# Optimization experiments

Hardware: AMD Instinct MI355X
Metric: run time of the kernel (lower is better)

Reference implementation:

```python
import jax, jax.numpy as jnp
import numpy as np

B, S, D, H = 128, 200, 512, 8
DF = D // H  # per-head feature dim = 64
SCALE = np.float32(1.0 / np.sqrt(DF))
NEG_INF = np.float32(-1e32)


def setup_inputs() -> dict:
    key = jax.random.key(0)
    ks = jax.random.split(key, 8)
    xavier = np.float32(np.sqrt(6.0 / (D + D)))  # xavier_uniform_ bound for square Linear
    def lin_w(k):
        return jax.random.uniform(k, (D, D), jnp.float32, -xavier, xavier)
    return {
        "q": jax.random.normal(ks[0], (B, S, D), jnp.float32),
        "k": jax.random.normal(ks[1], (B, S, D), jnp.float32),
        "v": jax.random.normal(ks[2], (B, S, D), jnp.float32),
        "Wq": lin_w(ks[3]), "bq": jnp.zeros((D,), jnp.float32),
        "Wk": lin_w(ks[4]), "bk": jnp.zeros((D,), jnp.float32),
        "Wv": lin_w(ks[5]), "bv": jnp.zeros((D,), jnp.float32),
        "Wo": lin_w(ks[6]), "bo": jnp.zeros((D,), jnp.float32),
        # causal mask: attend only to positions <= query position
        "mask": jnp.tril(jnp.ones((1, 1, S, S), dtype=bool)),
        "zero_pad": 1,
    }


def reference(q, k, v, Wq, bq, Wk, bk, Wv, bv, Wo, bo, mask, zero_pad):
    bs, s, d = q.shape
    # QKV projections -> [B, H, S, DF]
    qh = (q @ Wq.T + bq).reshape(bs, s, H, DF).transpose(0, 2, 1, 3)
    kh = (k @ Wk.T + bk).reshape(bs, s, H, DF).transpose(0, 2, 1, 3)
    vh = (v @ Wv.T + bv).reshape(bs, s, H, DF).transpose(0, 2, 1, 3)
    # attention4dis_kt: scaled dot-product, causal mask fill with -1e32, softmax
    scores = jnp.einsum("bhqd,bhkd->bhqk", qh, kh) * SCALE
    scores = jnp.where(mask, scores, NEG_INF)
    attn = jax.nn.softmax(scores, axis=-1)  # [B, H, S, S]
    if zero_pad:
        # replace first query row of attention weights with zeros
        attn = attn.at[:, :, 0, :].set(0.0)
    # dropout is identity in eval mode
    out = jnp.einsum("bhqk,bhkd->bhqd", attn, vh)
    concat = out.transpose(0, 2, 1, 3).reshape(bs, s, d)
    return concat @ Wo.T + bo
```

## Files before the change

### kernel.cpp

```cpp
#include <hip/hip_runtime.h>
#include <hip/hip_bf16.h>

#define SEQ  200
#define DIM  512
#define NH   8
#define DF   64
#define SPAD 256
#define NEG  -1.0e30f

typedef __bf16 bf16x8 __attribute__((ext_vector_type(8)));
typedef __bf16 bf16x4 __attribute__((ext_vector_type(4)));
typedef float  f32x4  __attribute__((ext_vector_type(4)));

__device__ __forceinline__ void async_lds16(const void* g, void* l)
{
    __builtin_amdgcn_global_load_lds(
        (const __attribute__((address_space(1))) void*)g,
        (__attribute__((address_space(3))) void*)l, 16, 0, 0);
}

struct DetArgs { const unsigned short* p[11]; };

__global__ void detect_all(DetArgs a, int* __restrict__ flags)
{
    const unsigned short* __restrict__ src = a.p[blockIdx.x];
    __shared__ int cnt;
    if (threadIdx.x == 0) cnt = 0;
    __syncthreads();
    int ok = 0;
#pragma unroll
    for (int i = 0; i < 2; ++i) {
        const unsigned short u = src[threadIdx.x * 2 + i];
        const float f = __uint_as_float(((unsigned int)u) << 16);
        const float fa = fabsf(f);
        ok += (f == 0.0f) || (fa >= 6.0e-5f && fa <= 64.0f);
    }
    atomicAdd(&cnt, ok);
    __syncthreads();
    if (threadIdx.x == 0) flags[blockIdx.x] = (cnt < 448) ? 1 : 0;
}

struct CvtArgs { const void* src[8]; __bf16* dst[8]; };

__global__ void cvt_all(CvtArgs a, const int* __restrict__ flags)
{
    const int blk = blockIdx.x;
    int job; long idx, n8;
    if (blk < 512) { job = blk >> 7; idx = (long)(blk & 127) * 256 + threadIdx.x; n8 = (long)DIM * DIM / 8; }
    else           { job = 4 + (blk - 512); idx = threadIdx.x; n8 = DIM / 8; }
    if (idx >= n8) return;
    const int fl = flags[3 + job];
    if (fl) {
        const f32x4* s = (const f32x4*)a.src[job];
        const f32x4 x = s[2 * idx], y = s[2 * idx + 1];
        bf16x8 o;
        o[0] = (__bf16)x[0]; o[1] = (__bf16)x[1];
        o[2] = (__bf16)x[2]; o[3] = (__bf16)x[3];
        o[4] = (__bf16)y[0]; o[5] = (__bf16)y[1];
        o[6] = (__bf16)y[2]; o[7] = (__bf16)y[3];
        ((bf16x8*)a.dst[job])[idx] = o;
    } else {
        ((bf16x8*)a.dst[job])[idx] = ((const bf16x8*)a.src[job])[idx];
    }
}

template <int MODE, int USE_FLAG, typename OutT>
__global__ __launch_bounds__(256, 2)
void gemm_bt_kernel(const void* __restrict__ Araw, long m_off,
                    const __bf16* __restrict__ Bt,
                    const __bf16* __restrict__ bias,
                    OutT* __restrict__ C,
                    int M, int N, int K,
                    const int* __restrict__ flag)
{
    __shared__ __align__(16) __bf16 lA[2][128 * 32];
    __shared__ __align__(16) __bf16 lB[2][128 * 32];

    const int af32 = USE_FLAG ? flag[0] : 0;
    const __bf16* A16 = (const __bf16*)Araw;
    const float*  A32 = (const float*)Araw;

    const int tid  = threadIdx.x;
    const int m0   = blockIdx.x * 128;
    const int n0   = blockIdx.y * 128;
    const int w    = tid >> 6;
    const int lane = tid & 63;
    const int lr   = lane & 15, quad = lane >> 4;
    const int wm   = (w >> 1) * 64, wn = (w & 1) * 64;

    int srow[2], scol[2];
#pragma unroll
    for (int p = 0; p < 2; ++p) {
        const int e = (p * 256 + tid) * 8;
        srow[p] = e >> 5;
        scol[p] = e & 31;
    }

    const int KS = K >> 5;
    f32x4 rf[2][2];

#pragma unroll
    for (int p = 0; p < 2; ++p)
        async_lds16(Bt + (size_t)(n0 + srow[p]) * K + scol[p],
                    &lB[0][(p * 256 + tid) * 8]);
    if (af32) {
#pragma unroll
        for (int p = 0; p < 2; ++p) {
            const size_t aoff = (size_t)(m_off + m0 + srow[p]) * K + scol[p];
            rf[p][0] = *(const f32x4*)(A32 + aoff);
            rf[p][1] = *(const f32x4*)(A32 + aoff + 4);
        }
    } else {
#pragma unroll
        for (int p = 0; p < 2; ++p)
            async_lds16(A16 + (size_t)(m_off + m0 + srow[p]) * K + scol[p],
                        &lA[0][(p * 256 + tid) * 8]);
    }

    f32x4 acc[4][4] = {};

    for (int ks = 0; ks < KS; ++ks) {
        const int buf = ks & 1;

        if (af32) {
#pragma unroll
            for (int p = 0; p < 2; ++p) {
                bf16x8 o;
                o[0] = (__bf16)rf[p][0][0]; o[1] = (__bf16)rf[p][0][1];
                o[2] = (__bf16)rf[p][0][2]; o[3] = (__bf16)rf[p][0][3];
                o[4] = (__bf16)rf[p][1][0]; o[5] = (__bf16)rf[p][1][1];
                o[6] = (__bf16)rf[p][1][2]; o[7] = (__bf16)rf[p][1][3];
                *(bf16x8*)&lA[buf][(p * 256 + tid) * 8] = o;
            }
        }

        __syncthreads();

        if (ks + 1 < KS) {
            const int k1 = (ks + 1) * 32;
#pragma unroll
            for (int p = 0; p < 2; ++p)
                async_lds16(Bt + (size_t)(n0 + srow[p]) * K + k1 + scol[p],
                            &lB[buf ^ 1][(p * 256 + tid) * 8]);
            if (af32) {
#pragma unroll
                for (int p = 0; p < 2; ++p) {
                    const size_t aoff =
                        (size_t)(m_off + m0 + srow[p]) * K + k1 + scol[p];
                    rf[p][0] = *(const f32x4*)(A32 + aoff);
                    rf[p][1] = *(const f32x4*)(A32 + aoff + 4);
                }
            } else {
#pragma unroll
                for (int p = 0; p < 2; ++p)
                    async_lds16(A16 + (size_t)(m_off + m0 + srow[p]) * K + k1 + scol[p],
                                &lA[buf ^ 1][(p * 256 + tid) * 8]);
            }
        }

        bf16x8 af[4], bfr[4];
#pragma unroll
        for (int mi = 0; mi < 4; ++mi)
            af[mi] = *(const bf16x8*)&lA[buf][(wm + mi * 16 + lr) * 32 + quad * 8];
#pragma unroll
        for (int ni = 0; ni < 4; ++ni)
            bfr[ni] = *(const bf16x8*)&lB[buf][(wn + ni * 16 + lr) * 32 + quad * 8];
#pragma unroll
        for (int mi = 0; mi < 4; ++mi)
#pragma unroll
            for (int ni = 0; ni < 4; ++ni)
                acc[mi][ni] = __builtin_amdgcn_mfma_f32_16x16x32_bf16(
                    af[mi], bfr[ni], acc[mi][ni], 0, 0, 0);
    }

#pragma unroll
    for (int ni = 0; ni < 4; ++ni) {
        const int col = n0 + wn + ni * 16 + lr;
        const float bb = (float)bias[col];
        if constexpr (MODE == 2) {
            const int h = col >> 6, df = col & 63;
#pragma unroll
            for (int mi = 0; mi < 4; ++mi) {
                const int row0 = m0 + wm + mi * 16 + quad * 4;
                const int b = row0 / SEQ, s0 = row0 - b * SEQ;
                bf16x4 pk;
#pragma unroll
                for (int r = 0; r < 4; ++r)
                    pk[r] = (__bf16)(acc[mi][ni][r] + bb);
                *(bf16x4*)&C[(((size_t)(b * NH + h)) * DF + df) * SPAD + s0] = pk;
            }
        } else {
#pragma unroll
            for (int mi = 0; mi < 4; ++mi) {
#pragma unroll
                for (int r = 0; r < 4; ++r) {
                    const int row = m0 + wm + mi * 16 + quad * 4 + r;
                    const float vv = acc[mi][ni][r] + bb;
                    size_t addr;
                    if (MODE == 0) {
                        addr = (size_t)row * N + col;
                    } else {
                        const int b = row / SEQ, s = row - b * SEQ;
                        const int h = col >> 6, df = col & 63;
                        addr = (((size_t)(b * NH + h)) * SEQ + s) * DF + df;
                    }
                    C[addr] = (OutT)vv;
                }
            }
        }
    }
}

#define KROWS 208
#define KSTR  72
#define VSTR  232
#define PSTR  136

__global__ __launch_bounds__(256, 2)
void attn_mfma(const __bf16* __restrict__ Qh,
               const __bf16* __restrict__ Kh,
               const __bf16* __restrict__ Vt,
               __bf16* __restrict__ Ctx,
               const int* __restrict__ zp)
{
    __shared__ __align__(16) __bf16 Kl[KROWS * KSTR];
    __shared__ __align__(16) __bf16 Vl[DF * VSTR];
    __shared__ __align__(16) __bf16 Pl[4][16 * PSTR];

    const int tid  = threadIdx.x;
    const int w    = tid >> 6, lane = tid & 63;
    const int lr   = lane & 15, quad = lane >> 4;
    const int bh   = blockIdx.x;
    const int b    = bh >> 3, h = bh & 7;
    const size_t qkbase = (size_t)bh * SEQ * DF;
    const size_t vbase  = (size_t)bh * DF * SPAD;
    const int zero_pad = zp[0];

    for (int i = tid; i < (KROWS * DF) / 8; i += 256) {
        const int row = i >> 3, c8 = (i & 7) * 8;
        *(bf16x8*)&Kl[row * KSTR + c8] =
            *(const bf16x8*)(Kh + qkbase + (size_t)row * DF + c8);
    }
    for (int i = tid; i < (DF * 224) / 8; i += 256) {
        const int d = i / 28, kb = (i % 28) * 8;
        bf16x8 vv = {};
        if (kb < SEQ)
            vv = *(const bf16x8*)(Vt + vbase + (size_t)d * SPAD + kb);
        *(bf16x8*)&Vl[d * VSTR + kb] = vv;
    }
    __syncthreads();

    __bf16* pw = Pl[w];

    const unsigned int mine =
        (unsigned int)(0x0459F38AF17BF26CULL >> (16 * w)) & 0xFFFFu;

    for (int j = 0; j < 4; ++j) {
        const int qt = (mine >> (4 * j)) & 15;
        if (qt == 15) continue;
        const int q = qt * 16 + lr;

        bf16x8 qf0, qf1;
        {
            const __bf16* qp = Qh + qkbase + (size_t)(qt * 16 + lr) * DF + quad * 8;
            qf0 = *(const bf16x8*)qp;
            qf1 = *(const bf16x8*)(qp + 32);
        }

        f32x4 sc[14];
#pragma unroll
        for (int kt = 0; kt < 13; ++kt) {
            if (kt > qt) continue;
            const int krow = kt * 16 + lr;
            const bf16x8 kf0 = *(const bf16x8*)&Kl[krow * KSTR + quad * 8];
            const bf16x8 kf1 = *(const bf16x8*)&Kl[krow * KSTR + 32 + quad * 8];
            f32x4 z = {};
            z = __builtin_amdgcn_mfma_f32_16x16x32_bf16(kf0, qf0, z, 0, 0, 0);
            z = __builtin_amdgcn_mfma_f32_16x16x32_bf16(kf1, qf1, z, 0, 0, 0);
            sc[kt] = z;
        }

        float mx = NEG;
#pragma unroll
        for (int kt = 0; kt < 13; ++kt) {
            if (kt > qt) continue;
#pragma unroll
            for (int r = 0; r < 4; ++r) {
                const int kk = kt * 16 + quad * 4 + r;
                const float s = (kk <= q && kk < SEQ) ? sc[kt][r] * 0.125f : NEG;
                sc[kt][r] = s;
                mx = fmaxf(mx, s);
            }
        }
        mx = fmaxf(mx, __shfl_xor(mx, 16, 64));
        mx = fmaxf(mx, __shfl_xor(mx, 32, 64));

        float l = 0.0f;
#pragma unroll
        for (int kt = 0; kt < 13; ++kt) {
            if (kt > qt) continue;
#pragma unroll
            for (int r = 0; r < 4; ++r) {
                const float pv = __expf(sc[kt][r] - mx);
                sc[kt][r] = pv;
                l += pv;
            }
        }
        l += __shfl_xor(l, 16, 64);
        l += __shfl_xor(l, 32, 64);
        const float linv = 1.0f / l;

        f32x4 oacc[4] = {};

#pragma unroll
        for (int kt = 0; kt < 8; ++kt) {
            if (kt <= qt) {
                bf16x4 pkv;
#pragma unroll
                for (int r = 0; r < 4; ++r) pkv[r] = (__bf16)sc[kt][r];
                *(bf16x4*)&pw[lr * PSTR + kt * 16 + quad * 4] = pkv;
            } else if (kt == qt + 1) {
                *(bf16x4*)&pw[lr * PSTR + kt * 16 + quad * 4] = (bf16x4){};
            }
        }
#pragma unroll
        for (int c = 0; c < 4; ++c) {
            if (2 * c > qt) continue;
            const bf16x8 pf = *(const bf16x8*)&pw[lr * PSTR + c * 32 + quad * 8];
#pragma unroll
            for (int nt = 0; nt < 4; ++nt) {
                const bf16x8 vf =
                    *(const bf16x8*)&Vl[(nt * 16 + lr) * VSTR + c * 32 + quad * 8];
                oacc[nt] = __builtin_amdgcn_mfma_f32_16x16x32_bf16(
                    pf, vf, oacc[nt], 0, 0, 0);
            }
        }

        if (qt >= 8) {
#pragma unroll
            for (int kt = 8; kt < 14; ++kt) {
                if (kt <= qt) {
                    bf16x4 pkv;
#pragma unroll
                    for (int r = 0; r < 4; ++r) pkv[r] = (__bf16)sc[kt][r];
                    *(bf16x4*)&pw[lr * PSTR + (kt - 8) * 16 + quad * 4] = pkv;
                } else if (kt == qt + 1) {
                    *(bf16x4*)&pw[lr * PSTR + (kt - 8) * 16 + quad * 4] = (bf16x4){};
                }
            }
#pragma unroll
            for (int c = 0; c < 3; ++c) {
                if (2 * (c + 4) > qt) continue;
                const bf16x8 pf = *(const bf16x8*)&pw[lr * PSTR + c * 32 + quad * 8];
#pragma unroll
                for (int nt = 0; nt < 4; ++nt) {
                    const bf16x8 vf =
                        *(const bf16x8*)&Vl[(nt * 16 + lr) * VSTR + (c + 4) * 32 + quad * 8];
                    oacc[nt] = __builtin_amdgcn_mfma_f32_16x16x32_bf16(
                        pf, vf, oacc[nt], 0, 0, 0);
                }
            }
        }

        float il[4];
#pragma unroll
        for (int r = 0; r < 4; ++r) il[r] = __shfl(linv, quad * 4 + r, 16);
#pragma unroll
        for (int nt = 0; nt < 4; ++nt) {
            const int d = nt * 16 + lr;
#pragma unroll
            for (int r = 0; r < 4; ++r) {
                const int qq = qt * 16 + quad * 4 + r;
                if (qq < SEQ) {
                    float ov = oacc[nt][r] * il[r];
                    if (zero_pad && qq == 0) ov = 0.0f;
                    Ctx[((size_t)(b * SEQ + qq)) * DIM + h * DF + d] = (__bf16)ov;
                }
            }
        }
    }
}

extern "C" void kernel_launch(void* const* d_in, const int* in_sizes, int n_in,
                              void* d_out, int out_size, void* d_ws, size_t ws_size,
                              hipStream_t stream)
{
    const void* q  = d_in[0];
    const void* k  = d_in[1];
    const void* v  = d_in[2];
    const void* Ws[4] = {d_in[3], d_in[5], d_in[7], d_in[9]};
    const void* bs[4] = {d_in[4], d_in[6], d_in[8], d_in[10]};
    const int*  zp = (const int*)d_in[12];
    float* Out = (float*)d_out;

    int* flags = (int*)d_ws;
    __bf16* Wc[4]; __bf16* bc[4];
    __bf16* p = (__bf16*)((char*)d_ws + 256);
    for (int i = 0; i < 4; ++i) { Wc[i] = p; p += (size_t)DIM * DIM; }
    for (int i = 0; i < 4; ++i) { bc[i] = p; p += DIM; }
    const size_t fixed_bytes = (size_t)((char*)p - (char*)d_ws);

    const int B_total = 128;
    int cb = 128;
    while (cb > 16) {
        const size_t crows_t = (size_t)cb * SEQ;
        const size_t elems = 4 * crows_t * DIM + (size_t)cb * NH * DF * SPAD;
        if (fixed_bytes + elems * 2 <= ws_size) break;
        cb >>= 1;
    }
    const int nchunk = B_total / cb;
    const size_t crows = (size_t)cb * SEQ;
    const size_t celems = crows * DIM;

    __bf16* Qh  = p;
    __bf16* Kh  = Qh + celems;
    __bf16* Vt  = Kh + celems;
    __bf16* Ctx = Vt + (size_t)cb * NH * DF * SPAD;

    const dim3 blk(256);
    const dim3 g((unsigned)(crows / 128), DIM / 128);

    DetArgs da;
    da.p[0] = (const unsigned short*)q;
    da.p[1] = (const unsigned short*)k;
    da.p[2] = (const unsigned short*)v;
    for (int i = 0; i < 4; ++i) {
        da.p[3 + i] = (const unsigned short*)Ws[i];
        da.p[7 + i] = (const unsigned short*)bs[i];
    }
    detect_all<<<dim3(11), blk, 0, stream>>>(da, flags);

    CvtArgs ca;
    for (int i = 0; i < 4; ++i) {
        ca.src[i] = Ws[i];     ca.dst[i] = Wc[i];
        ca.src[4 + i] = bs[i]; ca.dst[4 + i] = bc[i];
    }
    cvt_all<<<dim3(516), blk, 0, stream>>>(ca, flags);

    for (int c = 0; c < nchunk; ++c) {
        const long moff = (long)c * (long)crows;
        gemm_bt_kernel<1, 1, __bf16><<<g, blk, 0, stream>>>(
            q, moff, Wc[0], bc[0], Qh, (int)crows, DIM, DIM, &flags[0]);
        gemm_bt_kernel<1, 1, __bf16><<<g, blk, 0, stream>>>(
            k, moff, Wc[1], bc[1], Kh, (int)crows, DIM, DIM, &flags[1]);
        gemm_bt_kernel<2, 1, __bf16><<<g, blk, 0, stream>>>(
            v, moff, Wc[2], bc[2], Vt, (int)crows, DIM, DIM, &flags[2]);
        attn_mfma<<<dim3(cb * NH), blk, 0, stream>>>(Qh, Kh, Vt, Ctx, zp);
        gemm_bt_kernel<0, 0, float><<<g, blk, 0, stream>>>(
            Ctx, 0, Wc[3], bc[3], Out + (size_t)c * celems,
            (int)crows, DIM, DIM, nullptr);
    }
}
```

Baseline: 329.7 us.

## Drop K staging in LDS and stream P in small chunks to raise occupancy

Removes the shared-memory copy of K. The attention kernel now reads K fragments straight from global memory, relying on L1/L2 caching across waves. It also replaces the large per-wave P buffer with a 16x40 buffer that is refilled for each 32-column chunk, which shrinks LDS use enough to raise the launch bound to 4 blocks per CU. The trade-off is more global/L2 traffic and latency for K, which is reread by up to 4 waves, plus more LDS write/read round trips per chunk.

```diff
diff --git a/kernel.cpp b/kernel.cpp
--- a/kernel.cpp
+++ b/kernel.cpp
@@ -211,21 +211,18 @@
     }
 }
 
-#define KROWS 208
-#define KSTR  72
 #define VSTR  232
-#define PSTR  136
-
-__global__ __launch_bounds__(256, 2)
+#define PSTRW 40
+
+__global__ __launch_bounds__(256, 4)
 void attn_mfma(const __bf16* __restrict__ Qh,
                const __bf16* __restrict__ Kh,
                const __bf16* __restrict__ Vt,
                __bf16* __restrict__ Ctx,
                const int* __restrict__ zp)
 {
-    __shared__ __align__(16) __bf16 Kl[KROWS * KSTR];
     __shared__ __align__(16) __bf16 Vl[DF * VSTR];
-    __shared__ __align__(16) __bf16 Pl[4][16 * PSTR];
+    __shared__ __align__(16) __bf16 Pl[4][16 * PSTRW];
 
     const int tid  = threadIdx.x;
     const int w    = tid >> 6, lane = tid & 63;
@@ -236,11 +233,6 @@
     const size_t vbase  = (size_t)bh * DF * SPAD;
     const int zero_pad = zp[0];
 
-    for (int i = tid; i < (KROWS * DF) / 8; i += 256) {
-        const int row = i >> 3, c8 = (i & 7) * 8;
-        *(bf16x8*)&Kl[row * KSTR + c8] =
-            *(const bf16x8*)(Kh + qkbase + (size_t)row * DF + c8);
-    }
     for (int i = tid; i < (DF * 224) / 8; i += 256) {
         const int d = i / 28, kb = (i % 28) * 8;
         bf16x8 vv = {};
@@ -267,13 +259,13 @@
             qf1 = *(const bf16x8*)(qp + 32);
         }
 
-        f32x4 sc[14];
+        f32x4 sc[13];
 #pragma unroll
         for (int kt = 0; kt < 13; ++kt) {
             if (kt > qt) continue;
-            const int krow = kt * 16 + lr;
-            const bf16x8 kf0 = *(const bf16x8*)&Kl[krow * KSTR + quad * 8];
-            const bf16x8 kf1 = *(const bf16x8*)&Kl[krow * KSTR + 32 + quad * 8];
+            const __bf16* kp = Kh + qkbase + (size_t)(kt * 16 + lr) * DF + quad * 8;
+            const bf16x8 kf0 = *(const bf16x8*)kp;
+            const bf16x8 kf1 = *(const bf16x8*)(kp + 32);
             f32x4 z = {};
             z = __builtin_amdgcn_mfma_f32_16x16x32_bf16(kf0, qf0, z, 0, 0, 0);
             z = __builtin_amdgcn_mfma_f32_16x16x32_bf16(kf1, qf1, z, 0, 0, 0);
@@ -311,54 +303,28 @@
         const float linv = 1.0f / l;
 
         f32x4 oacc[4] = {};
-
-#pragma unroll
-        for (int kt = 0; kt < 8; ++kt) {
-            if (kt <= qt) {
-                bf16x4 pkv;
-#pragma unroll
-                for (int r = 0; r < 4; ++r) pkv[r] = (__bf16)sc[kt][r];
-                *(bf16x4*)&pw[lr * PSTR + kt * 16 + quad * 4] = pkv;
-            } else if (kt == qt + 1) {
-                *(bf16x4*)&pw[lr * PSTR + kt * 16 + quad * 4] = (bf16x4){};
-            }
-        }
-#pragma unroll
-        for (int c = 0; c < 4; ++c) {
+#pragma unroll
+        for (int c = 0; c < 7; ++c) {
             if (2 * c > qt) continue;
-            const bf16x8 pf = *(const bf16x8*)&pw[lr * PSTR + c * 32 + quad * 8];
+#pragma unroll
+            for (int tt = 0; tt < 2; ++tt) {
+                const int t = 2 * c + tt;
+                if (t <= qt) {
+                    bf16x4 pkv;
+#pragma unroll
+                    for (int r = 0; r < 4; ++r) pkv[r] = (__bf16)sc[t][r];
+                    *(bf16x4*)&pw[lr * PSTRW + tt * 16 + quad * 4] = pkv;
+                } else if (t == qt + 1) {
+                    *(bf16x4*)&pw[lr * PSTRW + tt * 16 + quad * 4] = (bf16x4){};
+                }
+            }
+            const bf16x8 pf = *(const bf16x8*)&pw[lr * PSTRW + quad * 8];
 #pragma unroll
             for (int nt = 0; nt < 4; ++nt) {
                 const bf16x8 vf =
                     *(const bf16x8*)&Vl[(nt * 16 + lr) * VSTR + c * 32 + quad * 8];
                 oacc[nt] = __builtin_amdgcn_mfma_f32_16x16x32_bf16(
                     pf, vf, oacc[nt], 0, 0, 0);
-            }
-        }
-
-        if (qt >= 8) {
-#pragma unroll
-            for (int kt = 8; kt < 14; ++kt) {
-                if (kt <= qt) {
-                    bf16x4 pkv;
-#pragma unroll
-                    for (int r = 0; r < 4; ++r) pkv[r] = (__bf16)sc[kt][r];
-                    *(bf16x4*)&pw[lr * PSTR + (kt - 8) * 16 + quad * 4] = pkv;
-                } else if (kt == qt + 1) {
-                    *(bf16x4*)&pw[lr * PSTR + (kt - 8) * 16 + quad * 4] = (bf16x4){};
-                }
-            }
-#pragma unroll
-            for (int c = 0; c < 3; ++c) {
-                if (2 * (c + 4) > qt) continue;
-                const bf16x8 pf = *(const bf16x8*)&pw[lr * PSTR + c * 32 + quad * 8];
-#pragma unroll
-                for (int nt = 0; nt < 4; ++nt) {
-                    const bf16x8 vf =
-                        *(const bf16x8*)&Vl[(nt * 16 + lr) * VSTR + (c + 4) * 32 + quad * 8];
-                    oacc[nt] = __builtin_amdgcn_mfma_f32_16x16x32_bf16(
-                        pf, vf, oacc[nt], 0, 0, 0);
-                }
             }
         }
 
```

Result: no change. 336.1 us (+2.0%).
